# Performance work log

Hardware: AMD Instinct MI355X
Metric: run time of the kernel (lower is better)

## Reference

```python
import jax, jax.numpy as jnp
import numpy as np

IN_FEATURES = 256
OUT_FEATURES = 256
INTERNAL = (IN_FEATURES + OUT_FEATURES) // 2  # trajectron AdditiveAttention default


def setup_inputs() -> dict:
    key = jax.random.key(0)
    k1, k2, k3, k4, k5 = jax.random.split(key, 5)
    B, TH, TQ = 32, 256, 64
    inputs = jax.random.normal(k1, (B, TH, IN_FEATURES), dtype=jnp.float32)
    state = jax.random.normal(k2, (B, TQ, OUT_FEATURES), dtype=jnp.float32)
    # Linear weights (no bias), Kaiming-ish scale
    w1 = jax.random.normal(k3, (INTERNAL, IN_FEATURES), dtype=jnp.float32) / np.sqrt(IN_FEATURES)
    w2 = jax.random.normal(k4, (INTERNAL, OUT_FEATURES), dtype=jnp.float32) / np.sqrt(OUT_FEATURES)
    v = jax.random.normal(k5, (INTERNAL,), dtype=jnp.float32) / np.sqrt(INTERNAL)
    return {"inputs": inputs, "state": state, "w1": w1, "w2": w2, "v": v, "batch_size": B}


def reference(inputs, state, w1, w2, v, batch_size):
    # history annotations: (B, Th, Din); future annotations (queries): (B, Tq, Dout)
    keys = inputs.reshape(batch_size, -1, IN_FEATURES)
    queries = state.reshape(batch_size, -1, OUT_FEATURES)
    # Additive (Bahdanau) attention: score = v . tanh(W1 k + W2 q)
    k_proj = jnp.einsum('bti,di->btd', keys, w1)       # (B, Th, D)
    q_proj = jnp.einsum('bqo,do->bqd', queries, w2)    # (B, Tq, D)
    scores = jnp.einsum('d,bqtd->bqt', v, jnp.tanh(q_proj[:, :, None, :] + k_proj[:, None, :, :]))
    alpha = jax.nn.softmax(scores, axis=-1)            # softmax over history axis
    contexts = jnp.einsum('bqt,bti->bqi', alpha, keys)  # (B, Tq, Din)
    # reshape + dropout (eval mode / p effectively 0 -> identity)
    return contexts.reshape(-1, IN_FEATURES)
```

## Files before the change

kernel.cpp:

```cpp
#include <hip/hip_runtime.h>
#include <math.h>

#define BATCH 32
#define TH    256
#define TQn   64
#define DIN   256
#define DD    256
#define QT    4
#define E2C   2.885390081777927f
#define DENMAX 1.0e9f

typedef __attribute__((ext_vector_type(8)))  short bf16x8;
typedef __attribute__((ext_vector_type(16))) float floatx16;

__device__ __forceinline__ float readlane_f(float x, int l) {
    return __int_as_float(__builtin_amdgcn_readlane(__float_as_int(x), l));
}

__device__ __forceinline__ float eclamp(float x) {
    return __builtin_amdgcn_exp2f(fminf(x * E2C, 30.f));
}

__device__ __forceinline__ void split2(float x0, float x1, unsigned& hi, unsigned& lo) {
    unsigned u0 = __float_as_uint(x0), u1 = __float_as_uint(x1);
    unsigned h0 = u0 & 0xFFFF0000u,   h1 = u1 & 0xFFFF0000u;
    float r0 = x0 - __uint_as_float(h0);
    float r1 = x1 - __uint_as_float(h1);
    hi = (u0 >> 16) | h1;
    lo = (__float_as_uint(r0) >> 16) | (__float_as_uint(r1) & 0xFFFF0000u);
}

__device__ __forceinline__ void split8(float4 f0, float4 f1, uint4& hi, uint4& lo) {
    split2(f0.x, f0.y, hi.x, lo.x);
    split2(f0.z, f0.w, hi.y, lo.y);
    split2(f1.x, f1.y, hi.z, lo.z);
    split2(f1.z, f1.w, hi.w, lo.w);
}

#define REG4  65
#define WOFF  (16 * REG4)
#define TSTR  68
__global__ __launch_bounds__(256, 4)
void proj_kernel(const float* __restrict__ keys,
                 const float* __restrict__ state,
                 const float* __restrict__ w1,
                 const float* __restrict__ w2,
                 float* __restrict__ ktp,
                 float* __restrict__ qpo)
{
    __shared__ uint4 lds4[2 * 16 * REG4];

    const int bid = blockIdx.x;
    const int tid = threadIdx.x;

    const float* X;
    const float* W;
    int m0, n0;
    bool is_kp;
    if (bid < 512) {
        is_kp = true;
        m0 = (bid >> 2) * 64;
        n0 = (bid & 3) * 64;
        X = keys; W = w1;
    } else {
        is_kp = false;
        int lb = bid - 512;
        m0 = (lb >> 2) * 64;
        n0 = (lb & 3) * 64;
        X = state; W = w2;
    }

    const int w    = tid >> 6;
    const int l    = tid & 63;
    const int mt   = w >> 1;
    const int nt   = w & 1;
    const int srow = tid >> 3;
    const int kg   = tid & 7;
    const int s_s  = kg >> 1;
    const int lidx = (srow & 31) + 32 * (kg & 1);

    floatx16 acc = {};

    for (int k0 = 0; k0 < DIN; k0 += 64) {
        #pragma unroll
        for (int hrow = 0; hrow < 2; hrow++) {
            int m = srow + hrow * 32;
            const float* px = X + (size_t)(m0 + m) * DIN + k0 + kg * 8;
            uint4 hi, lo;
            split8(*(const float4*)px, *(const float4*)(px + 4), hi, lo);
            int g = m >> 5;
            lds4[((0 * 2 + g) * 4 + s_s) * REG4 + lidx] = hi;
            lds4[((2 + g) * 4 + s_s) * REG4 + lidx] = lo;
            const float* pw = W + (size_t)(n0 + m) * DIN + k0 + kg * 8;
            split8(*(const float4*)pw, *(const float4*)(pw + 4), hi, lo);
            lds4[WOFF + ((0 * 2 + g) * 4 + s_s) * REG4 + lidx] = hi;
            lds4[WOFF + ((2 + g) * 4 + s_s) * REG4 + lidx] = lo;
        }
        __syncthreads();

        #pragma unroll
        for (int s = 0; s < 4; s++) {
            uint4 ahr = lds4[((0 * 2 + mt) * 4 + s) * REG4 + l];
            uint4 alr = lds4[((2 + mt) * 4 + s) * REG4 + l];
            uint4 bhr = lds4[WOFF + ((0 * 2 + nt) * 4 + s) * REG4 + l];
            uint4 blr = lds4[WOFF + ((2 + nt) * 4 + s) * REG4 + l];
            bf16x8 ah = __builtin_bit_cast(bf16x8, ahr);
            bf16x8 al = __builtin_bit_cast(bf16x8, alr);
            bf16x8 bh = __builtin_bit_cast(bf16x8, bhr);
            bf16x8 bl = __builtin_bit_cast(bf16x8, blr);
            acc = __builtin_amdgcn_mfma_f32_32x32x16_bf16(ah, bh, acc, 0, 0, 0);
            acc = __builtin_amdgcn_mfma_f32_32x32x16_bf16(al, bh, acc, 0, 0, 0);
            acc = __builtin_amdgcn_mfma_f32_32x32x16_bf16(ah, bl, acc, 0, 0, 0);
        }
        __syncthreads();
    }

    const int col = l & 31;
    const int hl  = l >> 5;
    if (is_kp) {
        float* sT = (float*)lds4;
        const int d_local = nt * 32 + col;
        #pragma unroll
        for (int r = 0; r < 16; r++) {
            int t_local = mt * 32 + 4 * hl + 8 * (r >> 2) + (r & 3);
            sT[t_local * TSTR + d_local] = eclamp(acc[r]);
        }
        __syncthreads();
        const int b  = m0 >> 8;
        const int t0 = m0 & 255;
        float4* dst4 = (float4*)ktp;
        #pragma unroll
        for (int p = 0; p < 4; p++) {
            int dp_local = w * 4 + p;
            float4 v4 = *(float4*)&sT[l * TSTR + dp_local * 4];
            dst4[(size_t)(b * 64 + (n0 >> 2) + dp_local) * 256 + t0 + l] = v4;
        }
    } else {
        const int d = n0 + nt * 32 + col;
        #pragma unroll
        for (int r = 0; r < 16; r++) {
            int row = (r & 3) + 8 * (r >> 2) + 4 * hl;
            qpo[(size_t)(m0 + mt * 32 + row) * DD + d] = eclamp(acc[r]);
        }
    }
}

__global__ __launch_bounds__(1024, 8)
void attn_kernel(const float* __restrict__ keys,
                 const float* __restrict__ vvec,
                 const float* __restrict__ ktp,
                 const float* __restrict__ qp,
                 float* __restrict__ out)
{
    __shared__ float s_part[4][QT][TH];
    __shared__ float s_alpha[QT][TH];
    __shared__ float s_rsum[QT];

    const int bid  = blockIdx.x;
    const int b    = bid & 31;
    const int q0   = (bid >> 5) * QT;
    const int tid  = threadIdx.x;
    const int t    = tid & 255;
    const int dgu  = __builtin_amdgcn_readfirstlane(tid >> 8);
    const int lane = tid & 63;
    const int wv   = tid >> 6;

    float acc[QT];
    #pragma unroll
    for (int q = 0; q < QT; q++) acc[q] = 0.f;

    const float4* kb4 = (const float4*)ktp + ((size_t)(b * 64 + dgu * 16) * 256 + t);
    const float*  qpb = qp + (size_t)(b * TQn + q0) * DD + dgu * 64;
    const float*  vv  = vvec + dgu * 64;

    #pragma unroll 4
    for (int dp = 0; dp < 16; dp++) {
        float4 kv = kb4[(size_t)dp * 256];
        float4 v4 = *(const float4*)(vv + dp * 4);
        #pragma unroll
        for (int q = 0; q < QT; q++) {
            float4 pq = *(const float4*)(qpb + q * DD + dp * 4);
            float d0 = fminf(fmaf(pq.x, kv.x, 1.f), DENMAX);
            float d1 = fminf(fmaf(pq.y, kv.y, 1.f), DENMAX);
            float d2 = fminf(fmaf(pq.z, kv.z, 1.f), DENMAX);
            float d3 = fminf(fmaf(pq.w, kv.w, 1.f), DENMAX);
            float n01 = fmaf(v4.y, d0, v4.x * d1);
            float d01 = d0 * d1;
            float n23 = fmaf(v4.w, d2, v4.z * d3);
            float d23 = d2 * d3;
            float num = fmaf(n23, d01, n01 * d23);
            float den = d01 * d23;
            acc[q] = fmaf(num, __builtin_amdgcn_rcpf(den), acc[q]);
        }
    }

    #pragma unroll
    for (int q = 0; q < QT; q++) s_part[dgu][q][t] = acc[q];
    __syncthreads();

    if (wv < QT) {
        const int q = wv;
        float x0, x1, x2, x3;
        {
            float p0 = s_part[0][q][lane]       + s_part[1][q][lane]
                     + s_part[2][q][lane]       + s_part[3][q][lane];
            float p1 = s_part[0][q][lane + 64]  + s_part[1][q][lane + 64]
                     + s_part[2][q][lane + 64]  + s_part[3][q][lane + 64];
            float p2 = s_part[0][q][lane + 128] + s_part[1][q][lane + 128]
                     + s_part[2][q][lane + 128] + s_part[3][q][lane + 128];
            float p3 = s_part[0][q][lane + 192] + s_part[1][q][lane + 192]
                     + s_part[2][q][lane + 192] + s_part[3][q][lane + 192];
            x0 = -2.f * p0; x1 = -2.f * p1; x2 = -2.f * p2; x3 = -2.f * p3;
        }
        float m = fmaxf(fmaxf(x0, x1), fmaxf(x2, x3));
        #pragma unroll
        for (int off = 32; off >= 1; off >>= 1) m = fmaxf(m, __shfl_xor(m, off));
        float e0 = __expf(x0 - m), e1 = __expf(x1 - m);
        float e2 = __expf(x2 - m), e3 = __expf(x3 - m);
        s_alpha[q][lane]       = e0;
        s_alpha[q][lane + 64]  = e1;
        s_alpha[q][lane + 128] = e2;
        s_alpha[q][lane + 192] = e3;
        float s = (e0 + e1) + (e2 + e3);
        #pragma unroll
        for (int off = 32; off >= 1; off >>= 1) s += __shfl_xor(s, off);
        if (lane == 0) s_rsum[q] = 1.f / s;
    }
    __syncthreads();

    float ctx[QT];
    #pragma unroll
    for (int q = 0; q < QT; q++) ctx[q] = 0.f;

    const float* krow = keys + ((size_t)b * TH + dgu * 64) * DIN + t;
    float ar[QT];
    #pragma unroll
    for (int q = 0; q < QT; q++) ar[q] = s_alpha[q][dgu * 64 + lane];

    for (int l = 0; l < 64; l += 4) {
        float kv4[4];
        #pragma unroll
        for (int j = 0; j < 4; j++)
            kv4[j] = krow[(size_t)(l + j) * DIN];
        #pragma unroll
        for (int j = 0; j < 4; j++) {
            #pragma unroll
            for (int q = 0; q < QT; q++)
                ctx[q] = fmaf(readlane_f(ar[q], l + j), kv4[j], ctx[q]);
        }
    }

    #pragma unroll
    for (int q = 0; q < QT; q++) s_part[dgu][q][t] = ctx[q];
    __syncthreads();

    {
        int q = tid >> 8, ii = tid & 255;
        float s = s_part[0][q][ii] + s_part[1][q][ii]
                + s_part[2][q][ii] + s_part[3][q][ii];
        out[(size_t)(b * TQn + q0 + q) * DIN + ii] = s * s_rsum[q];
    }
}

extern "C" void kernel_launch(void* const* d_in, const int* in_sizes, int n_in,
                              void* d_out, int out_size, void* d_ws, size_t ws_size,
                              hipStream_t stream) {
    (void)in_sizes; (void)n_in; (void)out_size; (void)ws_size;
    const float* keys  = (const float*)d_in[0];
    const float* state = (const float*)d_in[1];
    const float* w1    = (const float*)d_in[2];
    const float* w2    = (const float*)d_in[3];
    const float* v     = (const float*)d_in[4];
    float* out = (float*)d_out;

    float* ktp = (float*)d_ws;
    float* qp  = ktp + (size_t)BATCH * DD * TH;

    hipLaunchKernelGGL(proj_kernel, dim3(640), dim3(256), 0, stream,
                       keys, state, w1, w2, ktp, qp);
    hipLaunchKernelGGL(attn_kernel, dim3(BATCH * (TQn / QT)), dim3(1024), 0, stream,
                       keys, v, ktp, qp, out);
}
```

Before: 118.1 us.

## Restructure score loop with pairwise rcp and register prefetch, vectorize context GEMV

```diff
diff --git a/kernel.cpp b/kernel.cpp
--- a/kernel.cpp
+++ b/kernel.cpp
@@ -8,14 +8,10 @@
 #define DD    256
 #define QT    4
 #define E2C   2.885390081777927f
-#define DENMAX 1.0e9f
 
 typedef __attribute__((ext_vector_type(8)))  short bf16x8;
 typedef __attribute__((ext_vector_type(16))) float floatx16;
-
-__device__ __forceinline__ float readlane_f(float x, int l) {
-    return __int_as_float(__builtin_amdgcn_readlane(__float_as_int(x), l));
-}
+typedef __attribute__((ext_vector_type(4)))  float f32x4;
 
 __device__ __forceinline__ float eclamp(float x) {
     return __builtin_amdgcn_exp2f(fminf(x * E2C, 30.f));
@@ -170,28 +166,44 @@
     for (int q = 0; q < QT; q++) acc[q] = 0.f;
 
     const float4* kb4 = (const float4*)ktp + ((size_t)(b * 64 + dgu * 16) * 256 + t);
-    const float*  qpb = qp + (size_t)(b * TQn + q0) * DD + dgu * 64;
-    const float*  vv  = vvec + dgu * 64;
-
-    #pragma unroll 4
-    for (int dp = 0; dp < 16; dp++) {
-        float4 kv = kb4[(size_t)dp * 256];
-        float4 v4 = *(const float4*)(vv + dp * 4);
-        #pragma unroll
-        for (int q = 0; q < QT; q++) {
-            float4 pq = *(const float4*)(qpb + q * DD + dp * 4);
-            float d0 = fminf(fmaf(pq.x, kv.x, 1.f), DENMAX);
-            float d1 = fminf(fmaf(pq.y, kv.y, 1.f), DENMAX);
-            float d2 = fminf(fmaf(pq.z, kv.z, 1.f), DENMAX);
-            float d3 = fminf(fmaf(pq.w, kv.w, 1.f), DENMAX);
-            float n01 = fmaf(v4.y, d0, v4.x * d1);
-            float d01 = d0 * d1;
-            float n23 = fmaf(v4.w, d2, v4.z * d3);
-            float d23 = d2 * d3;
-            float num = fmaf(n23, d01, n01 * d23);
-            float den = d01 * d23;
-            acc[q] = fmaf(num, __builtin_amdgcn_rcpf(den), acc[q]);
-        }
+    const float* pqr0 = qp + (size_t)(b * TQn + q0 + 0) * DD + dgu * 64;
+    const float* pqr1 = qp + (size_t)(b * TQn + q0 + 1) * DD + dgu * 64;
+    const float* pqr2 = qp + (size_t)(b * TQn + q0 + 2) * DD + dgu * 64;
+    const float* pqr3 = qp + (size_t)(b * TQn + q0 + 3) * DD + dgu * 64;
+    const float* vvp  = vvec + dgu * 64;
+
+    float4 kv0 = kb4[0 * 256], kv1 = kb4[1 * 256],
+           kv2 = kb4[2 * 256], kv3 = kb4[3 * 256];
+
+    #pragma unroll
+    for (int c = 0; c < 4; c++) {
+        float4 n0v, n1v, n2v, n3v;
+        if (c < 3) {
+            const float4* p = kb4 + (size_t)(c + 1) * 4 * 256;
+            n0v = p[0 * 256]; n1v = p[1 * 256];
+            n2v = p[2 * 256]; n3v = p[3 * 256];
+        }
+        #pragma unroll
+        for (int u = 0; u < 4; u++) {
+            const int dp = c * 4 + u;
+            float4 kv = (u == 0) ? kv0 : (u == 1) ? kv1 : (u == 2) ? kv2 : kv3;
+            const float v0 = vvp[dp * 4 + 0], v1 = vvp[dp * 4 + 1];
+            const float v2 = vvp[dp * 4 + 2], v3 = vvp[dp * 4 + 3];
+            const float* pqr[QT] = {pqr0, pqr1, pqr2, pqr3};
+            #pragma unroll
+            for (int q = 0; q < QT; q++) {
+                const float* pr = pqr[q];
+                float d0 = fmaf(pr[dp * 4 + 0], kv.x, 1.f);
+                float d1 = fmaf(pr[dp * 4 + 1], kv.y, 1.f);
+                float n01 = fmaf(v1, d0, v0 * d1);
+                acc[q] = fmaf(n01, __builtin_amdgcn_rcpf(d0 * d1), acc[q]);
+                float d2 = fmaf(pr[dp * 4 + 2], kv.z, 1.f);
+                float d3 = fmaf(pr[dp * 4 + 3], kv.w, 1.f);
+                float n23 = fmaf(v3, d2, v2 * d3);
+                acc[q] = fmaf(n23, __builtin_amdgcn_rcpf(d2 * d3), acc[q]);
+            }
+        }
+        if (c < 3) { kv0 = n0v; kv1 = n1v; kv2 = n2v; kv3 = n3v; }
     }
 
     #pragma unroll
@@ -228,37 +240,48 @@
     }
     __syncthreads();
 
-    float ctx[QT];
-    #pragma unroll
-    for (int q = 0; q < QT; q++) ctx[q] = 0.f;
-
-    const float* krow = keys + ((size_t)b * TH + dgu * 64) * DIN + t;
-    float ar[QT];
-    #pragma unroll
-    for (int q = 0; q < QT; q++) ar[q] = s_alpha[q][dgu * 64 + lane];
-
-    for (int l = 0; l < 64; l += 4) {
-        float kv4[4];
-        #pragma unroll
-        for (int j = 0; j < 4; j++)
-            kv4[j] = krow[(size_t)(l + j) * DIN];
-        #pragma unroll
-        for (int j = 0; j < 4; j++) {
+    {
+        const int iqg = __builtin_amdgcn_readfirstlane((tid >> 6) & 3);
+        const int il  = lane & 15;
+        const int tl  = lane >> 4;
+        const int iq  = iqg * 16 + il;
+
+        f32x4 ctx4[QT] = {};
+        const float* kp0 = keys + ((size_t)b * TH + dgu * 64 + tl) * DIN + iq * 4;
+
+        #pragma unroll 4
+        for (int step = 0; step < 16; step++) {
+            f32x4 key4 = *(const f32x4*)(kp0 + (size_t)step * 4 * DIN);
+            const int ta = dgu * 64 + step * 4 + tl;
             #pragma unroll
             for (int q = 0; q < QT; q++)
-                ctx[q] = fmaf(readlane_f(ar[q], l + j), kv4[j], ctx[q]);
-        }
-    }
-
-    #pragma unroll
-    for (int q = 0; q < QT; q++) s_part[dgu][q][t] = ctx[q];
+                ctx4[q] += key4 * s_alpha[q][ta];
+        }
+
+        #pragma unroll
+        for (int q = 0; q < QT; q++) {
+            #pragma unroll
+            for (int k = 0; k < 4; k++) {
+                ctx4[q][k] += __shfl_xor(ctx4[q][k], 16);
+                ctx4[q][k] += __shfl_xor(ctx4[q][k], 32);
+            }
+        }
+        if (tl == 0) {
+            #pragma unroll
+            for (int q = 0; q < QT; q++)
+                *(f32x4*)&s_part[dgu][q][iq * 4] = ctx4[q];
+        }
+    }
     __syncthreads();
 
-    {
-        int q = tid >> 8, ii = tid & 255;
-        float s = s_part[0][q][ii] + s_part[1][q][ii]
-                + s_part[2][q][ii] + s_part[3][q][ii];
-        out[(size_t)(b * TQn + q0 + q) * DIN + ii] = s * s_rsum[q];
+    if (tid < 256) {
+        const int q = tid >> 6, iqf = tid & 63;
+        f32x4 s = *(const f32x4*)&s_part[0][q][iqf * 4];
+        s += *(const f32x4*)&s_part[1][q][iqf * 4];
+        s += *(const f32x4*)&s_part[2][q][iqf * 4];
+        s += *(const f32x4*)&s_part[3][q][iqf * 4];
+        s *= s_rsum[q];
+        *(f32x4*)&out[(size_t)(b * TQn + q0 + q) * DIN + iqf * 4] = s;
     }
 }
 
```

New measurement: 104.4 us. 1.13x faster.
